# Kernel tuning notes

Measured on AMD Instinct MI355X. Metric: run time of the kernel, lower is better.

The kernel has to match this reference:

```python
import jax, jax.numpy as jnp
import numpy as np

N, L, F, C, H, QK, Vd, Pq, Pv = 1, 512, 128, 64, 12, 32, 32, 8, 8


def _l2g(R, t, p):
    # p: (N,L,...,3) local -> global: R @ p + t
    o = jnp.einsum('nlij,nl...j->nl...i', R, p)
    return o + t.reshape(t.shape[0], t.shape[1], *((1,) * (p.ndim - 3)), 3)


def _g2l(R, t, q):
    # global -> local: R^T (q - t)
    d = q - t.reshape(t.shape[0], t.shape[1], *((1,) * (q.ndim - 3)), 3)
    return jnp.einsum('nlij,nl...i->nl...j', R, d)


def _ln(y, s, b, eps=1e-5):
    mu = y.mean(-1, keepdims=True)
    var = ((y - mu) ** 2).mean(-1, keepdims=True)
    return (y - mu) / jnp.sqrt(var + eps) * s + b


def setup_inputs() -> dict:
    key = jax.random.key(0)
    ks = jax.random.split(key, 16)
    sF = 1.0 / np.sqrt(F)
    sC = 1.0 / np.sqrt(C)
    cat = H * C + H * Vd + H * Pv * 3
    return {
        'R': jax.random.normal(ks[0], (N, L, 3, 3), jnp.float32),
        't': jax.random.normal(ks[1], (N, L, 3), jnp.float32),
        'x': jax.random.normal(ks[2], (N, L, F), jnp.float32),
        'z': jax.random.normal(ks[3], (N, L, L, C), jnp.float32),
        'mask': jnp.ones((N, L), dtype=bool),
        'Wq': jax.random.normal(ks[4], (F, H * QK), jnp.float32) * sF,
        'Wk': jax.random.normal(ks[5], (F, H * QK), jnp.float32) * sF,
        'Wpair': jax.random.normal(ks[6], (C, H), jnp.float32) * sC,
        'Wqp': jax.random.normal(ks[7], (F, H * Pq * 3), jnp.float32) * sF,
        'Wkp': jax.random.normal(ks[8], (F, H * Pq * 3), jnp.float32) * sF,
        'Wv': jax.random.normal(ks[9], (F, H * Vd), jnp.float32) * sF,
        'Wvp': jax.random.normal(ks[10], (F, H * Pv * 3), jnp.float32) * sF,
        'spatial_coef': jnp.full((1, 1, 1, H), np.log(np.e - 1.0), jnp.float32),
        'Wo': jax.random.normal(ks[11], (cat, F), jnp.float32) / np.sqrt(cat),
        'bo': jnp.zeros((F,), jnp.float32),
        'ln1_scale': jnp.ones((F,), jnp.float32),
        'ln1_offset': jnp.zeros((F,), jnp.float32),
        'W1': jax.random.normal(ks[12], (F, F), jnp.float32) * sF,
        'b1': jnp.zeros((F,), jnp.float32),
        'W2': jax.random.normal(ks[13], (F, F), jnp.float32) * sF,
        'b2': jnp.zeros((F,), jnp.float32),
        'W3': jax.random.normal(ks[14], (F, F), jnp.float32) * sF,
        'b3': jnp.zeros((F,), jnp.float32),
        'ln2_scale': jnp.ones((F,), jnp.float32),
        'ln2_offset': jnp.zeros((F,), jnp.float32),
    }


def reference(R, t, x, z, mask, Wq, Wk, Wpair, Wqp, Wkp, Wv, Wvp, spatial_coef,
              Wo, bo, ln1_scale, ln1_offset, W1, b1, W2, b2, W3, b3,
              ln2_scale, ln2_offset):
    # --- node logits ---
    q = (x @ Wq).reshape(N, L, H, QK)
    k = (x @ Wk).reshape(N, L, H, QK)
    logits_node = jnp.einsum('nihd,njhd->nijh', q, k) / np.float32(np.sqrt(QK))
    # --- pair logits ---
    logits_pair = z @ Wpair  # (N,L,L,H)
    # --- spatial logits ---
    qp = _l2g(R, t, (x @ Wqp).reshape(N, L, H * Pq, 3)).reshape(N, L, H, Pq * 3)
    kp = _l2g(R, t, (x @ Wkp).reshape(N, L, H * Pq, 3)).reshape(N, L, H, Pq * 3)
    q2 = (qp ** 2).sum(-1)  # (N,L,H)
    k2 = (kp ** 2).sum(-1)
    sum_sq_dist = q2[:, :, None] + k2[:, None] - 2.0 * jnp.einsum('nihd,njhd->nijh', qp, kp)
    gamma = jax.nn.softplus(spatial_coef)  # (1,1,1,H)
    logits_spatial = sum_sq_dist * (-gamma * np.float32(np.sqrt(2.0 / (9 * Pq))) / 2.0)
    # --- combine, mask, softmax ---
    logits = (logits_node + logits_pair + logits_spatial) * np.float32(np.sqrt(1.0 / 3.0))
    mask_pair = mask[:, :, None] & mask[:, None, :]  # (N,L,L)
    logits = jnp.where(mask_pair[..., None], logits, logits - 100000.0)
    alpha = jax.nn.softmax(logits, axis=2)
    alpha = jnp.where(mask[:, :, None, None], alpha, 0.0)
    # --- pair aggregation ---
    feat_p2n = jnp.einsum('nijh,nijc->nihc', alpha, z).reshape(N, L, H * C)
    # --- node aggregation ---
    v = (x @ Wv).reshape(N, L, H, Vd)
    feat_node = jnp.einsum('nijh,njhd->nihd', alpha, v).reshape(N, L, H * Vd)
    # --- spatial aggregation ---
    vp = _l2g(R, t, (x @ Wvp).reshape(N, L, H, Pv, 3))  # (N,L,H,Pv,3)
    aggr = jnp.einsum('nijh,njhpd->nihpd', alpha, vp)
    feat_points = _g2l(R, t, aggr)
    feat_spatial = feat_points.reshape(N, L, H * Pv * 3)
    # --- output transform + residual/LN + MLP ---
    feat_all = jnp.concatenate([feat_p2n, feat_node, feat_spatial], axis=-1) @ Wo + bo
    feat_all = jnp.where(mask[..., None], feat_all, 0.0)
    x1 = _ln(x + feat_all, ln1_scale, ln1_offset)
    h = jax.nn.relu(x1 @ W1 + b1)
    h = jax.nn.relu(h @ W2 + b2)
    mlp = h @ W3 + b3
    return _ln(x1 + mlp, ln2_scale, ln2_offset)
```

## Files before the change

### kernel.cpp

```cpp
#include <hip/hip_runtime.h>

#define PCOLS 2016

constexpr float INV_SQRT_QK = 0.17677669529663687f;
constexpr float S3          = 0.57735026918962576f;

#define FMA4(acc, s, b) { acc.x += (s)*(b).x; acc.y += (s)*(b).y; acc.z += (s)*(b).z; acc.w += (s)*(b).w; }
#define ADD4(acc, b)    { acc.x += (b).x; acc.y += (b).y; acc.z += (b).z; acc.w += (b).w; }

__global__ __launch_bounds__(256) void k1_gemm(
    const float* __restrict__ x,
    const float* __restrict__ Wq, const float* __restrict__ Wk,
    const float* __restrict__ Wqp, const float* __restrict__ Wkp,
    const float* __restrict__ Wv, const float* __restrict__ Wvp,
    float* __restrict__ proj) {
  int bt = blockIdx.x;
  int it = bt / 21, ot = bt % 21;
  int i0 = it * 64;
  int tid = threadIdx.x;
  int tr = tid >> 5, tc = tid & 31;
  __shared__ float xs[64 * 128];
  for (int idx = tid; idx < 8192; idx += 256) xs[idx] = x[i0 * 128 + idx];
  const float* Wsec; int lofs, width;
  if (ot < 4)       { Wsec = Wq;  lofs = ot * 96;        width = 384; }
  else if (ot < 8)  { Wsec = Wk;  lofs = (ot - 4) * 96;  width = 384; }
  else if (ot < 11) { Wsec = Wqp; lofs = (ot - 8) * 96;  width = 288; }
  else if (ot < 14) { Wsec = Wkp; lofs = (ot - 11) * 96; width = 288; }
  else if (ot < 18) { Wsec = Wv;  lofs = (ot - 14) * 96; width = 384; }
  else              { Wsec = Wvp; lofs = (ot - 18) * 96; width = 288; }
  __syncthreads();
  float acc[8][3];
  #pragma unroll
  for (int r = 0; r < 8; ++r) { acc[r][0] = 0.f; acc[r][1] = 0.f; acc[r][2] = 0.f; }
  const float* wp0 = Wsec + lofs + tc * 3;
  #pragma unroll 4
  for (int f = 0; f < 128; ++f) {
    float w0 = wp0[f * width], w1 = wp0[f * width + 1], w2 = wp0[f * width + 2];
    const float* xr = xs + (tr * 8) * 128 + f;
    #pragma unroll
    for (int r = 0; r < 8; ++r) {
      float xv = xr[r * 128];
      acc[r][0] += xv * w0; acc[r][1] += xv * w1; acc[r][2] += xv * w2;
    }
  }
  int gc = ot * 96 + tc * 3;
  #pragma unroll
  for (int r = 0; r < 8; ++r) {
    float* dst = proj + (size_t)(i0 + tr * 8 + r) * PCOLS + gc;
    dst[0] = acc[r][0]; dst[1] = acc[r][1]; dst[2] = acc[r][2];
  }
}

__global__ __launch_bounds__(256) void k1b_prep(
    const float* __restrict__ Rg, const float* __restrict__ tg, const float* __restrict__ sc,
    float* __restrict__ proj, float* __restrict__ Ac, float* __restrict__ Bc,
    float* __restrict__ a2, float* __restrict__ b2) {
  int j = blockIdx.x, tid = threadIdx.x;
  __shared__ float qk[1344];
  __shared__ float vps[288], Rs[9], ts[3], cf[12];
  float* pr = proj + (size_t)j * PCOLS;
  const float4* pr4 = (const float4*)pr;
  for (int g = tid; g < 336; g += 256) ((float4*)qk)[g] = pr4[g];
  for (int g = tid; g < 72; g += 256) ((float4*)vps)[g] = pr4[432 + g];
  if (tid < 9) Rs[tid] = Rg[j * 9 + tid];
  else if (tid < 12) ts[tid - 9] = tg[j * 3 + tid - 9];
  else if (tid < 24) cf[tid - 12] = -log1pf(__expf(sc[tid - 12])) * (1.0f / 12.0f);
  __syncthreads();
  for (int p = tid; p < 288; p += 256) {
    int sec = p / 96, m = p % 96;
    float* P = (sec == 0) ? qk + 768 : (sec == 1) ? qk + 1056 : vps;
    float* pp = P + m * 3;
    float p0 = pp[0], p1 = pp[1], p2 = pp[2];
    pp[0] = Rs[0]*p0 + Rs[1]*p1 + Rs[2]*p2 + ts[0];
    pp[1] = Rs[3]*p0 + Rs[4]*p1 + Rs[5]*p2 + ts[1];
    pp[2] = Rs[6]*p0 + Rs[7]*p1 + Rs[8]*p2 + ts[2];
  }
  __syncthreads();
  for (int g = tid; g < 72; g += 256) ((float4*)pr)[432 + g] = ((float4*)vps)[g];
  if (tid < 24) {
    int h = tid % 12;
    const float* s = (tid < 12) ? qk + 768 + h * 24 : qk + 1056 + h * 24;
    float a = 0.f;
    #pragma unroll
    for (int d = 0; d < 24; ++d) a += s[d] * s[d];
    float val = S3 * cf[h] * a;
    if (tid < 12) a2[h * 512 + j] = val; else b2[h * 512 + j] = val;
  }
  float s1 = S3 * INV_SQRT_QK;
  for (int o = tid; o < 672; o += 256) {
    int h = o / 56, d = o % 56;
    float s2 = -2.0f * S3 * cf[h];
    float aval = (d < 32) ? qk[h * 32 + d] * s1 : qk[768 + h * 24 + (d - 32)] * s2;
    float bval = (d < 32) ? qk[384 + h * 32 + d] : qk[1056 + h * 24 + (d - 32)];
    Ac[((size_t)h * 512 + j) * 56 + d] = aval;
    Bc[((size_t)h * 512 + j) * 56 + d] = bval;
  }
}

__global__ __launch_bounds__(256) void k2a_pair(
    const float* __restrict__ z, const float* __restrict__ Wpair,
    float* __restrict__ alphab) {
  int blk = blockIdx.x;
  int i = blk >> 2, j0 = (blk & 3) * 128;
  int tid = threadIdx.x;
  __shared__ float zt[128 * 68];
  __shared__ float wp[768];
  __shared__ float pl[12 * 128];
  if (tid < 192) ((float4*)wp)[tid] = ((const float4*)Wpair)[tid];
  const float4* zsrc = (const float4*)(z + ((size_t)i * 512 + j0) * 64);
  for (int g = tid; g < 2048; g += 256) {
    int row = g >> 4, c4 = g & 15;
    ((float4*)(zt + row * 68))[c4] = zsrc[row * 16 + c4];
  }
  __syncthreads();
  int jl = tid & 127, half = tid >> 7;
  float acc[12];
  #pragma unroll
  for (int h = 0; h < 12; ++h) acc[h] = 0.f;
  const float4* zr = (const float4*)(zt + jl * 68) + half * 8;
  #pragma unroll
  for (int c4 = 0; c4 < 8; ++c4) {
    float4 zv = zr[c4];
    const float* w0 = wp + (half * 8 + c4) * 48;
    #pragma unroll
    for (int h = 0; h < 12; ++h)
      acc[h] += zv.x * w0[h] + zv.y * w0[12 + h] + zv.z * w0[24 + h] + zv.w * w0[36 + h];
  }
  if (half == 1) {
    #pragma unroll
    for (int h = 0; h < 12; ++h) pl[h * 128 + jl] = acc[h];
  }
  __syncthreads();
  if (half == 0) {
    #pragma unroll
    for (int h = 0; h < 12; ++h)
      alphab[(size_t)h * 262144 + (size_t)i * 512 + j0 + jl] = (acc[h] + pl[h * 128 + jl]) * S3;
  }
}

__global__ __launch_bounds__(256) void k2b_logits(
    const float* __restrict__ Ac, const float* __restrict__ Bc,
    const float* __restrict__ a2, const float* __restrict__ b2,
    float* __restrict__ alphab) {
  int blk = blockIdx.x;
  int h = blk >> 5, i0 = (blk & 31) * 16;
  int tid = threadIdx.x;
  int ti = tid >> 5, tj = tid & 31;
  int r0 = 2 * ti;
  __shared__ float At[16 * 60];
  __shared__ float BtT[56 * 132];
  __shared__ float b2s[512];
  __shared__ float a2s[16];
  for (int g = tid; g < 224; g += 256) {
    int row = g / 14, u = g % 14;
    *(float4*)(At + row * 60 + u * 4) =
      *(const float4*)(Ac + ((size_t)h * 512 + i0 + row) * 56 + u * 4);
  }
  if (tid < 128) ((float4*)b2s)[tid] = ((const float4*)(b2 + h * 512))[tid];
  if (tid < 16) a2s[tid] = a2[h * 512 + i0 + tid];
  float lg[2][16];
  const size_t abase = (size_t)h * 262144;
  for (int jt = 0; jt < 4; ++jt) {
    int j0 = jt * 128;
    __syncthreads();
    for (int g = tid; g < 1792; g += 256) {
      int jl = g / 14, u = g % 14;
      float4 v = *(const float4*)(Bc + ((size_t)h * 512 + j0 + jl) * 56 + u * 4);
      BtT[(u * 4 + 0) * 132 + jl] = v.x;
      BtT[(u * 4 + 1) * 132 + jl] = v.y;
      BtT[(u * 4 + 2) * 132 + jl] = v.z;
      BtT[(u * 4 + 3) * 132 + jl] = v.w;
    }
    __syncthreads();
    float acc[2][4] = {{0.f,0.f,0.f,0.f},{0.f,0.f,0.f,0.f}};
    #pragma unroll 8
    for (int k = 0; k < 56; ++k) {
      float a0 = At[r0 * 60 + k], a1 = At[(r0 + 1) * 60 + k];
      float2 bA = *(const float2*)(BtT + k * 132 + 2 * tj);
      float2 bB = *(const float2*)(BtT + k * 132 + 64 + 2 * tj);
      acc[0][0] += a0 * bA.x; acc[0][1] += a0 * bA.y; acc[0][2] += a0 * bB.x; acc[0][3] += a0 * bB.y;
      acc[1][0] += a1 * bA.x; acc[1][1] += a1 * bA.y; acc[1][2] += a1 * bB.x; acc[1][3] += a1 * bB.y;
    }
    #pragma unroll
    for (int r = 0; r < 2; ++r) {
      int ig = i0 + r0 + r;
      const float* prow = alphab + abase + (size_t)ig * 512 + j0;
      int c0 = 2 * tj, c1 = 64 + 2 * tj;
      float arr = a2s[r0 + r];
      lg[r][jt*4+0] = acc[r][0] + prow[c0]     + arr + b2s[j0 + c0];
      lg[r][jt*4+1] = acc[r][1] + prow[c0 + 1] + arr + b2s[j0 + c0 + 1];
      lg[r][jt*4+2] = acc[r][2] + prow[c1]     + arr + b2s[j0 + c1];
      lg[r][jt*4+3] = acc[r][3] + prow[c1 + 1] + arr + b2s[j0 + c1 + 1];
    }
  }
  #pragma unroll
  for (int r = 0; r < 2; ++r) {
    float m = lg[r][0];
    #pragma unroll
    for (int u = 1; u < 16; ++u) m = fmaxf(m, lg[r][u]);
    #pragma unroll
    for (int s = 16; s > 0; s >>= 1) m = fmaxf(m, __shfl_xor(m, s));
    float ssum = 0.f;
    #pragma unroll
    for (int u = 0; u < 16; ++u) { lg[r][u] = __expf(lg[r][u] - m); ssum += lg[r][u]; }
    #pragma unroll
    for (int s = 16; s > 0; s >>= 1) ssum += __shfl_xor(ssum, s);
    float inv = 1.0f / ssum;
    float* orow = alphab + abase + (size_t)(i0 + r0 + r) * 512;
    #pragma unroll
    for (int jt = 0; jt < 4; ++jt) {
      *(float2*)(orow + jt * 128 + 2 * tj)      = make_float2(lg[r][jt*4+0] * inv, lg[r][jt*4+1] * inv);
      *(float2*)(orow + jt * 128 + 64 + 2 * tj) = make_float2(lg[r][jt*4+2] * inv, lg[r][jt*4+3] * inv);
    }
  }
}

__global__ __launch_bounds__(256) void k3a_p2n(
    const float* __restrict__ alphab, const float* __restrict__ z,
    float* __restrict__ featb) {
  int i = blockIdx.x, tid = threadIdx.x;
  __shared__ float al[12 * 516];
  __shared__ float zt[64 * 68];
  for (int g = tid; g < 1536; g += 256) {
    int row = g >> 7, c4 = g & 127;
    *(float4*)(al + row * 516 + c4 * 4) =
      *(const float4*)(alphab + (size_t)row * 262144 + (size_t)i * 512 + c4 * 4);
  }
  int h = tid >> 4, c4 = tid & 15;
  float4 acc = {0.f, 0.f, 0.f, 0.f};
  const float4* zsrc = (const float4*)(z + (size_t)i * 512 * 64);
  for (int t8 = 0; t8 < 8; ++t8) {
    __syncthreads();
    for (int g = tid; g < 1024; g += 256) {
      int row = g >> 4, cc = g & 15;
      *(float4*)(&zt[row * 68 + cc * 4]) = zsrc[(t8 * 64 + row) * 16 + cc];
    }
    __syncthreads();
    if (tid < 192) {
      const float* ar = al + h * 516 + t8 * 64;
      #pragma unroll
      for (int k4 = 0; k4 < 16; ++k4) {
        float4 a4 = *(const float4*)(&ar[k4 * 4]);
        float4 z0 = *(const float4*)(&zt[(k4*4+0) * 68 + c4 * 4]);
        float4 z1 = *(const float4*)(&zt[(k4*4+1) * 68 + c4 * 4]);
        float4 z2 = *(const float4*)(&zt[(k4*4+2) * 68 + c4 * 4]);
        float4 z3 = *(const float4*)(&zt[(k4*4+3) * 68 + c4 * 4]);
        FMA4(acc, a4.x, z0); FMA4(acc, a4.y, z1); FMA4(acc, a4.z, z2); FMA4(acc, a4.w, z3);
      }
    }
  }
  if (tid < 192)
    *(float4*)(&featb[(size_t)i * 1440 + h * 64 + c4 * 4]) = acc;
}

__global__ __launch_bounds__(256) void k3b_nodevp(
    const float* __restrict__ alphab, const float* __restrict__ proj,
    const float* __restrict__ Rg, const float* __restrict__ tg,
    float* __restrict__ featb) {
  int b = blockIdx.x;
  int h = b >> 4, it = b & 15, i0 = it * 32;
  int tid = threadIdx.x;
  __shared__ float At[32 * 68];
  __shared__ float Bt[64 * 60];
  __shared__ float ag[32 * 24];
  int cg = tid % 14, rg = tid / 14;
  int c0 = cg * 4, r0 = rg * 2;
  float4 acc0 = {0,0,0,0}, acc1 = {0,0,0,0};
  for (int t8 = 0; t8 < 8; ++t8) {
    int j0 = t8 * 64;
    __syncthreads();
    for (int g = tid; g < 512; g += 256) {
      int row = g >> 4, cc = g & 15;
      *(float4*)(&At[row * 68 + cc * 4]) =
        *(const float4*)(alphab + (size_t)h * 262144 + (size_t)(i0 + row) * 512 + j0 + cc * 4);
    }
    for (int g = tid; g < 896; g += 256) {
      int row = g / 14, u = g % 14;
      const float* pr = proj + (size_t)(j0 + row) * PCOLS;
      float4 vv = (u < 8) ? *(const float4*)(&pr[1344 + h * 32 + u * 4])
                          : *(const float4*)(&pr[1728 + h * 24 + (u - 8) * 4]);
      int dst = (u < 8) ? u * 4 : 32 + (u - 8) * 4;
      *(float4*)(&Bt[row * 60 + dst]) = vv;
    }
    __syncthreads();
    if (rg < 16) {
      #pragma unroll 4
      for (int kk = 0; kk < 64; kk += 4) {
        float4 a0 = *(const float4*)(&At[(r0+0) * 68 + kk]);
        float4 a1 = *(const float4*)(&At[(r0+1) * 68 + kk]);
        float4 b0 = *(const float4*)(&Bt[(kk+0) * 60 + c0]);
        float4 b1 = *(const float4*)(&Bt[(kk+1) * 60 + c0]);
        float4 b2v = *(const float4*)(&Bt[(kk+2) * 60 + c0]);
        float4 b3 = *(const float4*)(&Bt[(kk+3) * 60 + c0]);
        FMA4(acc0, a0.x, b0); FMA4(acc0, a0.y, b1); FMA4(acc0, a0.z, b2v); FMA4(acc0, a0.w, b3);
        FMA4(acc1, a1.x, b0); FMA4(acc1, a1.y, b1); FMA4(acc1, a1.z, b2v); FMA4(acc1, a1.w, b3);
      }
    }
  }
  __syncthreads();
  if (rg < 16) {
    #pragma unroll
    for (int r = 0; r < 2; ++r) {
      float4 v = (r == 0) ? acc0 : acc1;
      int row = r0 + r;
      if (c0 < 32) {
        *(float4*)(&featb[(size_t)(i0 + row) * 1440 + 768 + h * 32 + c0]) = v;
      } else {
        int cc = c0 - 32;
        ag[row * 24 + cc + 0] = v.x; ag[row * 24 + cc + 1] = v.y;
        ag[row * 24 + cc + 2] = v.z; ag[row * 24 + cc + 3] = v.w;
      }
    }
  }
  __syncthreads();
  {
    int row = tid >> 3, p = tid & 7;
    const float* R  = Rg + (size_t)(i0 + row) * 9;
    const float* tt = tg + (size_t)(i0 + row) * 3;
    float d0 = ag[row * 24 + p * 3 + 0] - tt[0];
    float d1 = ag[row * 24 + p * 3 + 1] - tt[1];
    float d2 = ag[row * 24 + p * 3 + 2] - tt[2];
    float* o = featb + (size_t)(i0 + row) * 1440 + 1152 + h * 24 + p * 3;
    o[0] = R[0]*d0 + R[3]*d1 + R[6]*d2;
    o[1] = R[1]*d0 + R[4]*d1 + R[7]*d2;
    o[2] = R[2]*d0 + R[5]*d1 + R[8]*d2;
  }
}

__global__ __launch_bounds__(512) void k4_mlp(
    const float* __restrict__ featb, const float* __restrict__ x,
    const float* __restrict__ Wo, const float* __restrict__ bo,
    const float* __restrict__ ln1s, const float* __restrict__ ln1o,
    const float* __restrict__ W1, const float* __restrict__ b1,
    const float* __restrict__ W2, const float* __restrict__ b2,
    const float* __restrict__ W3, const float* __restrict__ b3,
    const float* __restrict__ ln2s, const float* __restrict__ ln2o,
    float* __restrict__ out) {
  int i0 = blockIdx.x * 2;
  int tid = threadIdx.x;
  __shared__ float fs[2 * 1440];
  __shared__ float4 part4[16][2][32];
  __shared__ float stgA[2][128], stgB[2][128], stgC[2][128];
  for (int g = tid; g < 720; g += 512)
    ((float4*)fs)[g] = ((const float4*)(featb + (size_t)i0 * 1440))[g];
  __syncthreads();
  int q = tid >> 5, cg = tid & 31;
  {
    float4 a0 = {0,0,0,0}, a1 = {0,0,0,0};
    int cb = q * 90;
    const float* f0 = fs + cb, *f1 = fs + 1440 + cb;
    #pragma unroll 6
    for (int c = 0; c < 90; ++c) {
      float4 w = *((const float4*)(Wo + (size_t)(cb + c) * 128) + cg);
      FMA4(a0, f0[c], w);
      FMA4(a1, f1[c], w);
    }
    part4[q][0][cg] = a0;
    part4[q][1][cg] = a1;
  }
  __syncthreads();
  if (tid < 64) {
    int rr = tid >> 5, c = tid & 31;
    float4 s = part4[0][rr][c];
    #pragma unroll
    for (int k = 1; k < 16; ++k) ADD4(s, part4[k][rr][c]);
    float4 bo4 = ((const float4*)bo)[c];
    float4 xr4 = ((const float4*)(x + (size_t)(i0 + rr) * 128))[c];
    s.x += bo4.x + xr4.x; s.y += bo4.y + xr4.y; s.z += bo4.z + xr4.z; s.w += bo4.w + xr4.w;
    ((float4*)stgA[rr])[c] = s;
  }
  __syncthreads();
  int q2 = tid >> 7, col = tid & 127, rr = q2 & 1;
  float x1;
  {
    float y = stgA[rr][col];
    float s1 = 0.f, s2 = 0.f;
    #pragma unroll 8
    for (int c4 = 0; c4 < 32; ++c4) {
      float4 v = ((const float4*)stgA[rr])[c4];
      s1 += v.x + v.y + v.z + v.w;
      s2 += v.x*v.x + v.y*v.y + v.z*v.z + v.w*v.w;
    }
    float mu = s1 * (1.f / 128.f);
    float var = s2 * (1.f / 128.f) - mu * mu;
    x1 = (y - mu) * rsqrtf(var + 1e-5f) * ln1s[col] + ln1o[col];
  }
  __syncthreads();
  stgB[rr][col] = x1;
  __syncthreads();
  int sub = tid >> 5, rr1 = sub & 1, kq = sub >> 1;
  {
    float4 aa = {0,0,0,0};
    int c0 = kq * 16;
    #pragma unroll
    for (int c = 0; c < 16; ++c) {
      float4 w = *((const float4*)(W1 + (size_t)(c0 + c) * 128) + cg);
      FMA4(aa, stgB[rr1][c0 + c], w);
    }
    part4[sub][0][cg] = aa;
  }
  __syncthreads();
  if (tid < 64) {
    int r2 = tid >> 5, c = tid & 31;
    float4 s = part4[r2][0][c];
    #pragma unroll
    for (int k = 1; k < 8; ++k) ADD4(s, part4[k * 2 + r2][0][c]);
    float4 b4 = ((const float4*)b1)[c];
    s.x = fmaxf(s.x + b4.x, 0.f); s.y = fmaxf(s.y + b4.y, 0.f);
    s.z = fmaxf(s.z + b4.z, 0.f); s.w = fmaxf(s.w + b4.w, 0.f);
    ((float4*)stgA[r2])[c] = s;
  }
  __syncthreads();
  {
    float4 aa = {0,0,0,0};
    int c0 = kq * 16;
    #pragma unroll
    for (int c = 0; c < 16; ++c) {
      float4 w = *((const float4*)(W2 + (size_t)(c0 + c) * 128) + cg);
      FMA4(aa, stgA[rr1][c0 + c], w);
    }
    part4[sub][0][cg] = aa;
  }
  __syncthreads();
  if (tid < 64) {
    int r2 = tid >> 5, c = tid & 31;
    float4 s = part4[r2][0][c];
    #pragma unroll
    for (int k = 1; k < 8; ++k) ADD4(s, part4[k * 2 + r2][0][c]);
    float4 b4 = ((const float4*)b2)[c];
    s.x = fmaxf(s.x + b4.x, 0.f); s.y = fmaxf(s.y + b4.y, 0.f);
    s.z = fmaxf(s.z + b4.z, 0.f); s.w = fmaxf(s.w + b4.w, 0.f);
    ((float4*)stgC[r2])[c] = s;
  }
  __syncthreads();
  {
    float4 aa = {0,0,0,0};
    int c0 = kq * 16;
    #pragma unroll
    for (int c = 0; c < 16; ++c) {
      float4 w = *((const float4*)(W3 + (size_t)(c0 + c) * 128) + cg);
      FMA4(aa, stgC[rr1][c0 + c], w);
    }
    part4[sub][0][cg] = aa;
  }
  __syncthreads();
  if (tid < 64) {
    int r2 = tid >> 5, c = tid & 31;
    float4 s = part4[r2][0][c];
    #pragma unroll
    for (int k = 1; k < 8; ++k) ADD4(s, part4[k * 2 + r2][0][c]);
    float4 b4 = ((const float4*)b3)[c];
    s.x += b4.x; s.y += b4.y; s.z += b4.z; s.w += b4.w;
    ((float4*)stgA[r2])[c] = s;
  }
  __syncthreads();
  {
    float y2 = x1 + stgA[rr][col];
    stgC[rr][col] = y2;
    __syncthreads();
    float s1 = 0.f, s2 = 0.f;
    #pragma unroll 8
    for (int c4 = 0; c4 < 32; ++c4) {
      float4 v = ((const float4*)stgC[rr])[c4];
      s1 += v.x + v.y + v.z + v.w;
      s2 += v.x*v.x + v.y*v.y + v.z*v.z + v.w*v.w;
    }
    float mu = s1 * (1.f / 128.f);
    float var = s2 * (1.f / 128.f) - mu * mu;
    if (q2 < 2)
      out[(size_t)(i0 + rr) * 128 + col] = (y2 - mu) * rsqrtf(var + 1e-5f) * ln2s[col] + ln2o[col];
  }
}

extern "C" void kernel_launch(void* const* d_in, const int* in_sizes, int n_in,
                              void* d_out, int out_size, void* d_ws, size_t ws_size,
                              hipStream_t stream) {
  const float* Rg   = (const float*)d_in[0];
  const float* tg   = (const float*)d_in[1];
  const float* x    = (const float*)d_in[2];
  const float* z    = (const float*)d_in[3];
  const float* Wq   = (const float*)d_in[5];
  const float* Wk   = (const float*)d_in[6];
  const float* Wpair= (const float*)d_in[7];
  const float* Wqp  = (const float*)d_in[8];
  const float* Wkp  = (const float*)d_in[9];
  const float* Wv   = (const float*)d_in[10];
  const float* Wvp  = (const float*)d_in[11];
  const float* sc   = (const float*)d_in[12];
  const float* Wo   = (const float*)d_in[13];
  const float* bo   = (const float*)d_in[14];
  const float* ln1s = (const float*)d_in[15];
  const float* ln1o = (const float*)d_in[16];
  const float* W1   = (const float*)d_in[17];
  const float* b1   = (const float*)d_in[18];
  const float* W2   = (const float*)d_in[19];
  const float* b2   = (const float*)d_in[20];
  const float* W3   = (const float*)d_in[21];
  const float* b3   = (const float*)d_in[22];
  const float* ln2s = (const float*)d_in[23];
  const float* ln2o = (const float*)d_in[24];

  float* ws = (float*)d_ws;
  float* proj   = ws;
  float* Ac     = proj + 512 * 2016;
  float* Bc     = Ac + 344064;
  float* a2     = Bc + 344064;
  float* b2v    = a2 + 6144;
  float* alphab = b2v + 6144;
  float* featb  = alphab + 3145728;

  k1_gemm  <<<168, 256, 0, stream>>>(x, Wq, Wk, Wqp, Wkp, Wv, Wvp, proj);
  k1b_prep <<<512, 256, 0, stream>>>(Rg, tg, sc, proj, Ac, Bc, a2, b2v);
  k2a_pair <<<2048, 256, 0, stream>>>(z, Wpair, alphab);
  k2b_logits<<<384, 256, 0, stream>>>(Ac, Bc, a2, b2v, alphab);
  k3a_p2n  <<<512, 256, 0, stream>>>(alphab, z, featb);
  k3b_nodevp<<<192, 256, 0, stream>>>(alphab, proj, Rg, tg, featb);
  k4_mlp   <<<256, 512, 0, stream>>>(featb, x, Wo, bo, ln1s, ln1o,
                                     W1, b1, W2, b2, W3, b3, ln2s, ln2o, (float*)d_out);
}
```

Before: 141.9 us.

## Fuse node/point aggregation into logits kernel; retile projection GEMM; transpose Bc

The node-value and spatial-point aggregation kernel is folded into the softmax/logits kernel. The normalized alpha rows are kept in shared memory and multiplied against the value projections there, which removes one launch and the global re-read of alpha. Bc is now written transposed in the prep kernel so the logits kernel loads it with coalesced float4 reads instead of scattering a transpose into shared memory. The projection GEMM is retiled to 384 threads with the weights staged in shared memory and float4 outputs. The trade-off is that the fused kernel's second phase runs on only 384 blocks of 16 rows, versus 192 blocks of 32 rows before, so each block issues more proj loads and the available parallelism differs.

```diff
diff --git a/kernel.cpp b/kernel.cpp
--- a/kernel.cpp
+++ b/kernel.cpp
@@ -8,7 +8,7 @@
 #define FMA4(acc, s, b) { acc.x += (s)*(b).x; acc.y += (s)*(b).y; acc.z += (s)*(b).z; acc.w += (s)*(b).w; }
 #define ADD4(acc, b)    { acc.x += (b).x; acc.y += (b).y; acc.z += (b).z; acc.w += (b).w; }
 
-__global__ __launch_bounds__(256) void k1_gemm(
+__global__ __launch_bounds__(384) void k1_gemm(
     const float* __restrict__ x,
     const float* __restrict__ Wq, const float* __restrict__ Wk,
     const float* __restrict__ Wqp, const float* __restrict__ Wkp,
@@ -18,9 +18,8 @@
   int it = bt / 21, ot = bt % 21;
   int i0 = it * 64;
   int tid = threadIdx.x;
-  int tr = tid >> 5, tc = tid & 31;
   __shared__ float xs[64 * 128];
-  for (int idx = tid; idx < 8192; idx += 256) xs[idx] = x[i0 * 128 + idx];
+  __shared__ float ws[128 * 96];
   const float* Wsec; int lofs, width;
   if (ot < 4)       { Wsec = Wq;  lofs = ot * 96;        width = 384; }
   else if (ot < 8)  { Wsec = Wk;  lofs = (ot - 4) * 96;  width = 384; }
@@ -28,32 +27,36 @@
   else if (ot < 14) { Wsec = Wkp; lofs = (ot - 11) * 96; width = 288; }
   else if (ot < 18) { Wsec = Wv;  lofs = (ot - 14) * 96; width = 384; }
   else              { Wsec = Wvp; lofs = (ot - 18) * 96; width = 288; }
-  __syncthreads();
-  float acc[8][3];
-  #pragma unroll
-  for (int r = 0; r < 8; ++r) { acc[r][0] = 0.f; acc[r][1] = 0.f; acc[r][2] = 0.f; }
-  const float* wp0 = Wsec + lofs + tc * 3;
+  for (int g = tid; g < 2048; g += 384)
+    *(float4*)(xs + (g >> 5) * 128 + (g & 31) * 4) =
+      *(const float4*)(x + (size_t)(i0 + (g >> 5)) * 128 + (g & 31) * 4);
+  for (int g = tid; g < 3072; g += 384) {
+    int r = g / 24, u = g % 24;
+    *(float4*)(ws + r * 96 + u * 4) = *(const float4*)(Wsec + (size_t)r * width + lofs + u * 4);
+  }
+  __syncthreads();
+  int cg = tid % 24, tr = tid / 24;
+  float4 acc0 = {0,0,0,0}, acc1 = {0,0,0,0}, acc2 = {0,0,0,0}, acc3 = {0,0,0,0};
+  const float* x0 = xs + (tr * 4 + 0) * 128;
+  const float* x1 = xs + (tr * 4 + 1) * 128;
+  const float* x2 = xs + (tr * 4 + 2) * 128;
+  const float* x3 = xs + (tr * 4 + 3) * 128;
   #pragma unroll 4
-  for (int f = 0; f < 128; ++f) {
-    float w0 = wp0[f * width], w1 = wp0[f * width + 1], w2 = wp0[f * width + 2];
-    const float* xr = xs + (tr * 8) * 128 + f;
-    #pragma unroll
-    for (int r = 0; r < 8; ++r) {
-      float xv = xr[r * 128];
-      acc[r][0] += xv * w0; acc[r][1] += xv * w1; acc[r][2] += xv * w2;
-    }
-  }
-  int gc = ot * 96 + tc * 3;
-  #pragma unroll
-  for (int r = 0; r < 8; ++r) {
-    float* dst = proj + (size_t)(i0 + tr * 8 + r) * PCOLS + gc;
-    dst[0] = acc[r][0]; dst[1] = acc[r][1]; dst[2] = acc[r][2];
-  }
+  for (int k = 0; k < 128; ++k) {
+    float4 w = *(const float4*)(ws + k * 96 + cg * 4);
+    FMA4(acc0, x0[k], w); FMA4(acc1, x1[k], w);
+    FMA4(acc2, x2[k], w); FMA4(acc3, x3[k], w);
+  }
+  int gc = ot * 96 + cg * 4;
+  *(float4*)(proj + (size_t)(i0 + tr * 4 + 0) * PCOLS + gc) = acc0;
+  *(float4*)(proj + (size_t)(i0 + tr * 4 + 1) * PCOLS + gc) = acc1;
+  *(float4*)(proj + (size_t)(i0 + tr * 4 + 2) * PCOLS + gc) = acc2;
+  *(float4*)(proj + (size_t)(i0 + tr * 4 + 3) * PCOLS + gc) = acc3;
 }
 
 __global__ __launch_bounds__(256) void k1b_prep(
     const float* __restrict__ Rg, const float* __restrict__ tg, const float* __restrict__ sc,
-    float* __restrict__ proj, float* __restrict__ Ac, float* __restrict__ Bc,
+    float* __restrict__ proj, float* __restrict__ Ac, float* __restrict__ BcT,
     float* __restrict__ a2, float* __restrict__ b2) {
   int j = blockIdx.x, tid = threadIdx.x;
   __shared__ float qk[1344];
@@ -93,7 +96,7 @@
     float aval = (d < 32) ? qk[h * 32 + d] * s1 : qk[768 + h * 24 + (d - 32)] * s2;
     float bval = (d < 32) ? qk[384 + h * 32 + d] : qk[1056 + h * 24 + (d - 32)];
     Ac[((size_t)h * 512 + j) * 56 + d] = aval;
-    Bc[((size_t)h * 512 + j) * 56 + d] = bval;
+    BcT[((size_t)h * 56 + d) * 512 + j] = bval;
   }
 }
 
@@ -139,18 +142,23 @@
 }
 
 __global__ __launch_bounds__(256) void k2b_logits(
-    const float* __restrict__ Ac, const float* __restrict__ Bc,
+    const float* __restrict__ Ac, const float* __restrict__ BcT,
     const float* __restrict__ a2, const float* __restrict__ b2,
-    float* __restrict__ alphab) {
+    const float* __restrict__ proj, const float* __restrict__ Rg, const float* __restrict__ tg,
+    float* __restrict__ alphab, float* __restrict__ featb) {
   int blk = blockIdx.x;
   int h = blk >> 5, i0 = (blk & 31) * 16;
   int tid = threadIdx.x;
   int ti = tid >> 5, tj = tid & 31;
   int r0 = 2 * ti;
-  __shared__ float At[16 * 60];
-  __shared__ float BtT[56 * 132];
-  __shared__ float b2s[512];
-  __shared__ float a2s[16];
+  __shared__ float smem[12480];
+  float* At  = smem;
+  float* BtT = smem + 960;
+  float* b2s = smem + 8352;
+  float* a2s = smem + 8864;
+  float* als = smem;
+  float* Bt  = smem + 8256;
+  float* ag  = smem + 12096;
   for (int g = tid; g < 224; g += 256) {
     int row = g / 14, u = g % 14;
     *(float4*)(At + row * 60 + u * 4) =
@@ -164,12 +172,9 @@
     int j0 = jt * 128;
     __syncthreads();
     for (int g = tid; g < 1792; g += 256) {
-      int jl = g / 14, u = g % 14;
-      float4 v = *(const float4*)(Bc + ((size_t)h * 512 + j0 + jl) * 56 + u * 4);
-      BtT[(u * 4 + 0) * 132 + jl] = v.x;
-      BtT[(u * 4 + 1) * 132 + jl] = v.y;
-      BtT[(u * 4 + 2) * 132 + jl] = v.z;
-      BtT[(u * 4 + 3) * 132 + jl] = v.w;
+      int k = g >> 5, c4 = g & 31;
+      *(float4*)(BtT + k * 132 + c4 * 4) =
+        *(const float4*)(BcT + ((size_t)h * 56 + k) * 512 + j0 + c4 * 4);
     }
     __syncthreads();
     float acc[2][4] = {{0.f,0.f,0.f,0.f},{0.f,0.f,0.f,0.f}};
@@ -193,6 +198,7 @@
       lg[r][jt*4+3] = acc[r][3] + prow[c1 + 1] + arr + b2s[j0 + c1 + 1];
     }
   }
+  __syncthreads();
   #pragma unroll
   for (int r = 0; r < 2; ++r) {
     float m = lg[r][0];
@@ -206,12 +212,65 @@
     #pragma unroll
     for (int s = 16; s > 0; s >>= 1) ssum += __shfl_xor(ssum, s);
     float inv = 1.0f / ssum;
-    float* orow = alphab + abase + (size_t)(i0 + r0 + r) * 512;
+    int row = r0 + r;
+    float* orow = alphab + abase + (size_t)(i0 + row) * 512;
     #pragma unroll
     for (int jt = 0; jt < 4; ++jt) {
-      *(float2*)(orow + jt * 128 + 2 * tj)      = make_float2(lg[r][jt*4+0] * inv, lg[r][jt*4+1] * inv);
-      *(float2*)(orow + jt * 128 + 64 + 2 * tj) = make_float2(lg[r][jt*4+2] * inv, lg[r][jt*4+3] * inv);
-    }
+      float2 vA = make_float2(lg[r][jt*4+0] * inv, lg[r][jt*4+1] * inv);
+      float2 vB = make_float2(lg[r][jt*4+2] * inv, lg[r][jt*4+3] * inv);
+      *(float2*)(orow + jt * 128 + 2 * tj)      = vA;
+      *(float2*)(orow + jt * 128 + 64 + 2 * tj) = vB;
+      *(float2*)(als + row * 516 + jt * 128 + 2 * tj)      = vA;
+      *(float2*)(als + row * 516 + jt * 128 + 64 + 2 * tj) = vB;
+    }
+  }
+  int cg2 = tid % 14, rg = tid / 14;
+  int c0 = cg2 * 4;
+  float4 acc4 = {0,0,0,0};
+  for (int t8 = 0; t8 < 8; ++t8) {
+    int j0 = t8 * 64;
+    __syncthreads();
+    for (int g = tid; g < 896; g += 256) {
+      int row = g / 14, u = g % 14;
+      const float* pr = proj + (size_t)(j0 + row) * PCOLS;
+      float4 vv = (u < 8) ? *(const float4*)(&pr[1344 + h * 32 + u * 4])
+                          : *(const float4*)(&pr[1728 + h * 24 + (u - 8) * 4]);
+      int dst = (u < 8) ? u * 4 : 32 + (u - 8) * 4;
+      *(float4*)(Bt + row * 60 + dst) = vv;
+    }
+    __syncthreads();
+    if (rg < 16) {
+      const float* arow = als + rg * 516 + j0;
+      #pragma unroll 8
+      for (int kk = 0; kk < 64; ++kk) {
+        float a = arow[kk];
+        float4 b = *(const float4*)(Bt + kk * 60 + c0);
+        FMA4(acc4, a, b);
+      }
+    }
+  }
+  __syncthreads();
+  if (rg < 16) {
+    if (c0 < 32) {
+      *(float4*)(&featb[(size_t)(i0 + rg) * 1440 + 768 + h * 32 + c0]) = acc4;
+    } else {
+      int cc = c0 - 32;
+      ag[rg * 24 + cc + 0] = acc4.x; ag[rg * 24 + cc + 1] = acc4.y;
+      ag[rg * 24 + cc + 2] = acc4.z; ag[rg * 24 + cc + 3] = acc4.w;
+    }
+  }
+  __syncthreads();
+  if (tid < 128) {
+    int row = tid >> 3, p = tid & 7;
+    const float* R  = Rg + (size_t)(i0 + row) * 9;
+    const float* tt = tg + (size_t)(i0 + row) * 3;
+    float d0 = ag[row * 24 + p * 3 + 0] - tt[0];
+    float d1 = ag[row * 24 + p * 3 + 1] - tt[1];
+    float d2 = ag[row * 24 + p * 3 + 2] - tt[2];
+    float* o = featb + (size_t)(i0 + row) * 1440 + 1152 + h * 24 + p * 3;
+    o[0] = R[0]*d0 + R[3]*d1 + R[6]*d2;
+    o[1] = R[1]*d0 + R[4]*d1 + R[7]*d2;
+    o[2] = R[2]*d0 + R[5]*d1 + R[8]*d2;
   }
 }
 
@@ -251,80 +310,6 @@
   }
   if (tid < 192)
     *(float4*)(&featb[(size_t)i * 1440 + h * 64 + c4 * 4]) = acc;
-}
-
-__global__ __launch_bounds__(256) void k3b_nodevp(
-    const float* __restrict__ alphab, const float* __restrict__ proj,
-    const float* __restrict__ Rg, const float* __restrict__ tg,
-    float* __restrict__ featb) {
-  int b = blockIdx.x;
-  int h = b >> 4, it = b & 15, i0 = it * 32;
-  int tid = threadIdx.x;
-  __shared__ float At[32 * 68];
-  __shared__ float Bt[64 * 60];
-  __shared__ float ag[32 * 24];
-  int cg = tid % 14, rg = tid / 14;
-  int c0 = cg * 4, r0 = rg * 2;
-  float4 acc0 = {0,0,0,0}, acc1 = {0,0,0,0};
-  for (int t8 = 0; t8 < 8; ++t8) {
-    int j0 = t8 * 64;
-    __syncthreads();
-    for (int g = tid; g < 512; g += 256) {
-      int row = g >> 4, cc = g & 15;
-      *(float4*)(&At[row * 68 + cc * 4]) =
-        *(const float4*)(alphab + (size_t)h * 262144 + (size_t)(i0 + row) * 512 + j0 + cc * 4);
-    }
-    for (int g = tid; g < 896; g += 256) {
-      int row = g / 14, u = g % 14;
-      const float* pr = proj + (size_t)(j0 + row) * PCOLS;
-      float4 vv = (u < 8) ? *(const float4*)(&pr[1344 + h * 32 + u * 4])
-                          : *(const float4*)(&pr[1728 + h * 24 + (u - 8) * 4]);
-      int dst = (u < 8) ? u * 4 : 32 + (u - 8) * 4;
-      *(float4*)(&Bt[row * 60 + dst]) = vv;
-    }
-    __syncthreads();
-    if (rg < 16) {
-      #pragma unroll 4
-      for (int kk = 0; kk < 64; kk += 4) {
-        float4 a0 = *(const float4*)(&At[(r0+0) * 68 + kk]);
-        float4 a1 = *(const float4*)(&At[(r0+1) * 68 + kk]);
-        float4 b0 = *(const float4*)(&Bt[(kk+0) * 60 + c0]);
-        float4 b1 = *(const float4*)(&Bt[(kk+1) * 60 + c0]);
-        float4 b2v = *(const float4*)(&Bt[(kk+2) * 60 + c0]);
-        float4 b3 = *(const float4*)(&Bt[(kk+3) * 60 + c0]);
-        FMA4(acc0, a0.x, b0); FMA4(acc0, a0.y, b1); FMA4(acc0, a0.z, b2v); FMA4(acc0, a0.w, b3);
-        FMA4(acc1, a1.x, b0); FMA4(acc1, a1.y, b1); FMA4(acc1, a1.z, b2v); FMA4(acc1, a1.w, b3);
-      }
-    }
-  }
-  __syncthreads();
-  if (rg < 16) {
-    #pragma unroll
-    for (int r = 0; r < 2; ++r) {
-      float4 v = (r == 0) ? acc0 : acc1;
-      int row = r0 + r;
-      if (c0 < 32) {
-        *(float4*)(&featb[(size_t)(i0 + row) * 1440 + 768 + h * 32 + c0]) = v;
-      } else {
-        int cc = c0 - 32;
-        ag[row * 24 + cc + 0] = v.x; ag[row * 24 + cc + 1] = v.y;
-        ag[row * 24 + cc + 2] = v.z; ag[row * 24 + cc + 3] = v.w;
-      }
-    }
-  }
-  __syncthreads();
-  {
-    int row = tid >> 3, p = tid & 7;
-    const float* R  = Rg + (size_t)(i0 + row) * 9;
-    const float* tt = tg + (size_t)(i0 + row) * 3;
-    float d0 = ag[row * 24 + p * 3 + 0] - tt[0];
-    float d1 = ag[row * 24 + p * 3 + 1] - tt[1];
-    float d2 = ag[row * 24 + p * 3 + 2] - tt[2];
-    float* o = featb + (size_t)(i0 + row) * 1440 + 1152 + h * 24 + p * 3;
-    o[0] = R[0]*d0 + R[3]*d1 + R[6]*d2;
-    o[1] = R[1]*d0 + R[4]*d1 + R[7]*d2;
-    o[2] = R[2]*d0 + R[5]*d1 + R[8]*d2;
-  }
 }
 
 __global__ __launch_bounds__(512) void k4_mlp(
@@ -503,18 +488,17 @@
   float* ws = (float*)d_ws;
   float* proj   = ws;
   float* Ac     = proj + 512 * 2016;
-  float* Bc     = Ac + 344064;
-  float* a2     = Bc + 344064;
+  float* BcT    = Ac + 344064;
+  float* a2     = BcT + 344064;
   float* b2v    = a2 + 6144;
   float* alphab = b2v + 6144;
   float* featb  = alphab + 3145728;
 
-  k1_gemm  <<<168, 256, 0, stream>>>(x, Wq, Wk, Wqp, Wkp, Wv, Wvp, proj);
-  k1b_prep <<<512, 256, 0, stream>>>(Rg, tg, sc, proj, Ac, Bc, a2, b2v);
+  k1_gemm  <<<168, 384, 0, stream>>>(x, Wq, Wk, Wqp, Wkp, Wv, Wvp, proj);
+  k1b_prep <<<512, 256, 0, stream>>>(Rg, tg, sc, proj, Ac, BcT, a2, b2v);
   k2a_pair <<<2048, 256, 0, stream>>>(z, Wpair, alphab);
-  k2b_logits<<<384, 256, 0, stream>>>(Ac, Bc, a2, b2v, alphab);
+  k2b_logits<<<384, 256, 0, stream>>>(Ac, BcT, a2, b2v, proj, Rg, tg, alphab, featb);
   k3a_p2n  <<<512, 256, 0, stream>>>(alphab, z, featb);
-  k3b_nodevp<<<192, 256, 0, stream>>>(alphab, proj, Rg, tg, featb);
   k4_mlp   <<<256, 512, 0, stream>>>(featb, x, Wo, bo, ln1s, ln1o,
                                      W1, b1, W2, b2, W3, b3, ln2s, ln2o, (float*)d_out);
 }
```

After: 129.8 us. -8.5%, faster.
